# Optimization experiments

Hardware: AMD Instinct MI355X
Metric: run time of the kernel (lower is better)

Reference implementation:

```python
import jax, jax.numpy as jnp
import numpy as np

N, K = 8192, 16          # nodes, neighbours per node
FEAT = 128               # size + 1 (attention input dim)
DIST = 128               # distance_size (query dim & block width)
H, D = 8, 128            # heads, per-head attention size
HID = 128                # MLP hidden size
SCALE = 1.0 / np.sqrt(D)


def _lin_init(k, i, o):
    return jax.random.normal(k, (i, o), jnp.float32) / np.sqrt(i)


def setup_inputs() -> dict:
    key = jax.random.key(0)
    ks = jax.random.split(key, 12)
    z = lambda n: jnp.zeros((n,), jnp.float32)
    return {
        "features": jax.random.normal(ks[0], (N, FEAT), jnp.float32),
        "distance_features": jax.random.normal(ks[1], (N, DIST), jnp.float32),
        "structure": jax.random.randint(ks[2], (N, K), 0, N, jnp.int32),
        # attention projections
        "Wq": _lin_init(ks[3], DIST, H * D), "bq": z(H * D),
        "Wk": _lin_init(ks[4], FEAT, H * D), "bk": z(H * D),
        "Wv": _lin_init(ks[5], FEAT, H * D), "bv": z(H * D),
        "Wo": _lin_init(ks[6], H * D, DIST), "bo": z(DIST),
        # local MLP: depth=3 hidden layers + output layer
        "W1": _lin_init(ks[7], DIST, HID), "b1": z(HID),
        "W2": _lin_init(ks[8], HID, HID), "b2": z(HID),
        "W3": _lin_init(ks[9], HID, HID), "b3": z(HID),
        "W4": _lin_init(ks[10], HID, DIST), "b4": z(DIST),
    }


def reference(features, distance_features, structure,
              Wq, bq, Wk, bk, Wv, bv, Wo, bo,
              W1, b1, W2, b2, W3, b3, W4, b4):
    # bn / local_bn are identity (batch_norm=False); dropout identity (eval)
    normed = distance_features

    # NeighbourDotMultiHeadAttention: queries from distance feats, K/V from node feats
    q = (normed @ Wq + bq).reshape(N, H, D)
    k = (features @ Wk + bk).reshape(N, H, D)
    v = (features @ Wv + bv).reshape(N, H, D)
    kg = k[structure]                                  # [N, K, H, D] neighbour keys
    vg = v[structure]                                  # [N, K, H, D] neighbour values
    logits = jnp.einsum('nhd,nkhd->nkh', q, kg) * SCALE
    attn = jax.nn.softmax(logits, axis=1)              # over K neighbours
    att = jnp.einsum('nkh,nkhd->nhd', attn, vg).reshape(N, H * D)
    att_out = att @ Wo + bo                            # [N, DIST]

    out = distance_features + att_out                  # residual 1

    # local MLP with relu activations
    h = jax.nn.relu(out @ W1 + b1)
    h = jax.nn.relu(h @ W2 + b2)
    h = jax.nn.relu(h @ W3 + b3)
    mlp = h @ W4 + b4

    return out + mlp                                   # residual 2
```

## Files before the change

kernel.cpp:

```cpp
#include <hip/hip_runtime.h>
#include <hip/hip_bf16.h>

typedef float f32x4 __attribute__((ext_vector_type(4)));
typedef short s16x8 __attribute__((ext_vector_type(8)));
typedef unsigned short u16;

#define N_NODES 8192
#define KNBR 16
#define SCALE 0.08838834764831845f

__device__ __forceinline__ float bf2f(u16 h) {
    unsigned v = ((unsigned)h) << 16;
    return __builtin_bit_cast(float, v);
}
__device__ __forceinline__ u16 f2bf(float f) {
    unsigned u = __builtin_bit_cast(unsigned, f);
    u += 0x7fffu + ((u >> 16) & 1u);
    return (u16)(u >> 16);
}

__global__ void prep_kernel(const float* __restrict__ feat, const float* __restrict__ dist,
                            const float* __restrict__ Wq, const float* __restrict__ Wk,
                            const float* __restrict__ Wv, const float* __restrict__ Wo,
                            const float* __restrict__ W1, const float* __restrict__ W2,
                            const float* __restrict__ W3, const float* __restrict__ W4,
                            const float* __restrict__ bq, const float* __restrict__ bk,
                            const float* __restrict__ bv,
                            u16* __restrict__ featb, u16* __restrict__ distb,
                            u16* __restrict__ Wqkvt, u16* __restrict__ Wot,
                            u16* __restrict__ Wmlpt, float* __restrict__ bqkv) {
    int gid = blockIdx.x * 256 + threadIdx.x;
    featb[gid] = f2bf(feat[gid]);
    distb[gid] = f2bf(dist[gid]);
    if (gid < 3072 * 128) {
        int col = gid >> 7, k = gid & 127;
        float v = (col < 1024) ? Wq[k * 1024 + col]
                : (col < 2048) ? Wk[k * 1024 + (col - 1024)]
                               : Wv[k * 1024 + (col - 2048)];
        Wqkvt[gid] = f2bf(v);
    }
    if (gid < 128 * 1024) {
        int col = gid >> 10, k = gid & 1023;
        Wot[gid] = f2bf(Wo[k * 128 + col]);
    }
    if (gid < 4 * 128 * 128) {
        int m = gid >> 14, r = gid & 16383;
        int col = r >> 7, k = r & 127;
        const float* Wm = (m == 0) ? W1 : (m == 1) ? W2 : (m == 2) ? W3 : W4;
        Wmlpt[gid] = f2bf(Wm[k * 128 + col]);
    }
    if (gid < 3072) {
        bqkv[gid] = (gid < 1024) ? bq[gid] : (gid < 2048) ? bk[gid - 1024] : bv[gid - 2048];
    }
}

__global__ __launch_bounds__(256) void qkv_gemm(const u16* __restrict__ featb,
                                                const u16* __restrict__ distb,
                                                const u16* __restrict__ Wqkvt,
                                                const float* __restrict__ bqkv,
                                                u16* __restrict__ qkvh) {
    const int rt = blockIdx.x, ct = blockIdx.y;
    const int w = threadIdx.x >> 6, l = threadIdx.x & 63;
    const int rbase = rt * 64 + w * 16;
    const int cbase = ct * 128;
    const u16* A = (cbase < 1024) ? distb : featb;

    const u16* arow = A + (size_t)(rbase + (l & 15)) * 128 + ((l >> 4) * 8);

    f32x4 acc[8];
#pragma unroll
    for (int i = 0; i < 8; i++) acc[i] = (f32x4){0.f, 0.f, 0.f, 0.f};

#pragma unroll
    for (int kk = 0; kk < 4; kk++) {
        s16x8 af = *(const s16x8*)(arow + kk * 32);
#pragma unroll
        for (int nf = 0; nf < 8; nf++) {
            const u16* bp = Wqkvt + (size_t)(cbase + nf * 16 + (l & 15)) * 128
                          + kk * 32 + ((l >> 4) * 8);
            s16x8 bf = *(const s16x8*)bp;
            acc[nf] = __builtin_amdgcn_mfma_f32_16x16x32_bf16(af, bf, acc[nf], 0, 0, 0);
        }
    }
#pragma unroll
    for (int nf = 0; nf < 8; nf++) {
        const int gcol = cbase + nf * 16 + (l & 15);
        const float bias = bqkv[gcol];
        const int s = gcol >> 10;
        const int c = gcol & 1023;
        const int head = c >> 7, d = c & 127;
#pragma unroll
        for (int r = 0; r < 4; r++) {
            const int grow = rbase + (l >> 4) * 4 + r;
            qkvh[((size_t)(s * 8 + head) * 8192 + grow) * 128 + d] = f2bf(acc[nf][r] + bias);
        }
    }
}

__global__ __launch_bounds__(256) void attn_kernel(const u16* __restrict__ qkvh,
                                                   const int* __restrict__ structure,
                                                   u16* __restrict__ attb) {
    const int head = blockIdx.x & 7, chunk = blockIdx.x >> 3;
    const int w = threadIdx.x >> 6, l = threadIdx.x & 63;
    const int ni = l >> 3, lh = l & 7;
    const int n = chunk * 32 + w * 8 + ni;

    const u16* qrow = qkvh + ((size_t)(0 * 8 + head) * 8192 + n) * 128 + lh * 16;
    float qf[16];
    {
        s16x8 q0 = *(const s16x8*)qrow;
        s16x8 q1 = *(const s16x8*)(qrow + 8);
#pragma unroll
        for (int t = 0; t < 8; t++) { qf[t] = bf2f((u16)q0[t]); qf[8 + t] = bf2f((u16)q1[t]); }
    }

    const int2 idx2 = ((const int2*)structure)[n * 8 + lh];

    const u16* kbase = qkvh + (size_t)(1 * 8 + head) * 8192 * 128;
    const u16* vbase = qkvh + (size_t)(2 * 8 + head) * 8192 * 128;

    float logit[16];
#pragma unroll
    for (int j = 0; j < 16; j++) {
        int idx = __shfl(j & 1 ? idx2.y : idx2.x, (ni << 3) | (j >> 1));
        const u16* krow = kbase + (size_t)idx * 128 + lh * 16;
        s16x8 k0 = *(const s16x8*)krow;
        s16x8 k1 = *(const s16x8*)(krow + 8);
        float s = 0.f;
#pragma unroll
        for (int t = 0; t < 8; t++) {
            s += qf[t] * bf2f((u16)k0[t]);
            s += qf[8 + t] * bf2f((u16)k1[t]);
        }
        s += __shfl_xor(s, 1);
        s += __shfl_xor(s, 2);
        s += __shfl_xor(s, 4);
        logit[j] = s * SCALE;
    }

    float m = logit[0];
#pragma unroll
    for (int j = 1; j < 16; j++) m = fmaxf(m, logit[j]);
    float sum = 0.f;
#pragma unroll
    for (int j = 0; j < 16; j++) { logit[j] = __expf(logit[j] - m); sum += logit[j]; }
    const float inv = 1.f / sum;

    float acc[16];
#pragma unroll
    for (int t = 0; t < 16; t++) acc[t] = 0.f;
#pragma unroll
    for (int j = 0; j < 16; j++) {
        int idx = __shfl(j & 1 ? idx2.y : idx2.x, (ni << 3) | (j >> 1));
        const u16* vrow = vbase + (size_t)idx * 128 + lh * 16;
        s16x8 v0 = *(const s16x8*)vrow;
        s16x8 v1 = *(const s16x8*)(vrow + 8);
        const float p = logit[j] * inv;
#pragma unroll
        for (int t = 0; t < 8; t++) {
            acc[t]     += p * bf2f((u16)v0[t]);
            acc[8 + t] += p * bf2f((u16)v1[t]);
        }
    }

    s16x8 o0, o1;
#pragma unroll
    for (int t = 0; t < 8; t++) { o0[t] = (short)f2bf(acc[t]); o1[t] = (short)f2bf(acc[8 + t]); }
    u16* orow = attb + (size_t)n * 1024 + head * 128 + lh * 16;
    *(s16x8*)orow = o0;
    *(s16x8*)(orow + 8) = o1;
}

__global__ __launch_bounds__(64) void out_mlp(const u16* __restrict__ attb,
                                              const u16* __restrict__ Wot,
                                              const u16* __restrict__ Wmlpt,
                                              const float* __restrict__ dist,
                                              const float* __restrict__ bo,
                                              const float* __restrict__ b1,
                                              const float* __restrict__ b2,
                                              const float* __restrict__ b3,
                                              const float* __restrict__ b4,
                                              float* __restrict__ out) {
    __shared__ __attribute__((aligned(16))) u16 act[2][16][136];
    const int l = threadIdx.x & 63;
    const int rbase = blockIdx.x * 16;

    f32x4 acc[8];
#pragma unroll
    for (int i = 0; i < 8; i++) acc[i] = (f32x4){0.f, 0.f, 0.f, 0.f};

    const u16* ap = attb + (size_t)(rbase + (l & 15)) * 1024 + ((l >> 4) * 8);
#pragma unroll 4
    for (int kk = 0; kk < 32; kk++) {
        s16x8 af = *(const s16x8*)(ap + kk * 32);
#pragma unroll
        for (int nf = 0; nf < 8; nf++) {
            const u16* bp = Wot + (size_t)(nf * 16 + (l & 15)) * 1024 + kk * 32 + ((l >> 4) * 8);
            s16x8 bf = *(const s16x8*)bp;
            acc[nf] = __builtin_amdgcn_mfma_f32_16x16x32_bf16(af, bf, acc[nf], 0, 0, 0);
        }
    }

    float outsave[8][4];
#pragma unroll
    for (int nf = 0; nf < 8; nf++) {
        const int gcol = nf * 16 + (l & 15);
        const float bv = bo[gcol];
#pragma unroll
        for (int r = 0; r < 4; r++) {
            const int rl = (l >> 4) * 4 + r;
            float v = acc[nf][r] + bv + dist[(size_t)(rbase + rl) * 128 + gcol];
            outsave[nf][r] = v;
            act[0][rl][gcol] = f2bf(v);
        }
    }

#pragma unroll
    for (int layer = 0; layer < 4; layer++) {
        const int rd = layer & 1, wr = (layer + 1) & 1;
        f32x4 macc[8];
#pragma unroll
        for (int i = 0; i < 8; i++) macc[i] = (f32x4){0.f, 0.f, 0.f, 0.f};
#pragma unroll
        for (int kk = 0; kk < 4; kk++) {
            s16x8 af = *(const s16x8*)&act[rd][l & 15][kk * 32 + ((l >> 4) * 8)];
#pragma unroll
            for (int nf = 0; nf < 8; nf++) {
                const u16* bp = Wmlpt + layer * 16384
                              + (size_t)(nf * 16 + (l & 15)) * 128 + kk * 32 + ((l >> 4) * 8);
                s16x8 bf = *(const s16x8*)bp;
                macc[nf] = __builtin_amdgcn_mfma_f32_16x16x32_bf16(af, bf, macc[nf], 0, 0, 0);
            }
        }
        const float* bias = (layer == 0) ? b1 : (layer == 1) ? b2 : (layer == 2) ? b3 : b4;
        if (layer < 3) {
#pragma unroll
            for (int nf = 0; nf < 8; nf++) {
                const int gcol = nf * 16 + (l & 15);
                const float bv = bias[gcol];
#pragma unroll
                for (int r = 0; r < 4; r++) {
                    const int rl = (l >> 4) * 4 + r;
                    act[wr][rl][gcol] = f2bf(fmaxf(macc[nf][r] + bv, 0.f));
                }
            }
        } else {
#pragma unroll
            for (int nf = 0; nf < 8; nf++) {
                const int gcol = nf * 16 + (l & 15);
                const float bv = bias[gcol];
#pragma unroll
                for (int r = 0; r < 4; r++) {
                    const int rl = (l >> 4) * 4 + r;
                    out[(size_t)(rbase + rl) * 128 + gcol] = outsave[nf][r] + macc[nf][r] + bv;
                }
            }
        }
    }
}

extern "C" void kernel_launch(void* const* d_in, const int* in_sizes, int n_in,
                              void* d_out, int out_size, void* d_ws, size_t ws_size,
                              hipStream_t stream) {
    const float* features = (const float*)d_in[0];
    const float* dist     = (const float*)d_in[1];
    const int*   structure= (const int*)d_in[2];
    const float* Wq = (const float*)d_in[3];  const float* bq = (const float*)d_in[4];
    const float* Wk = (const float*)d_in[5];  const float* bk = (const float*)d_in[6];
    const float* Wv = (const float*)d_in[7];  const float* bv = (const float*)d_in[8];
    const float* Wo = (const float*)d_in[9];  const float* bo = (const float*)d_in[10];
    const float* W1 = (const float*)d_in[11]; const float* b1 = (const float*)d_in[12];
    const float* W2 = (const float*)d_in[13]; const float* b2 = (const float*)d_in[14];
    const float* W3 = (const float*)d_in[15]; const float* b3 = (const float*)d_in[16];
    const float* W4 = (const float*)d_in[17]; const float* b4 = (const float*)d_in[18];
    float* out = (float*)d_out;

    u16* wsp   = (u16*)d_ws;
    u16* qkvh  = wsp;
    u16* attb  = qkvh  + (size_t)3 * 8 * 8192 * 128;
    u16* featb = attb  + (size_t)8192 * 1024;
    u16* distb = featb + (size_t)8192 * 128;
    u16* Wqkvt = distb + (size_t)8192 * 128;
    u16* Wot   = Wqkvt + (size_t)3072 * 128;
    u16* Wmlpt = Wot   + (size_t)128 * 1024;
    float* bqkv = (float*)(Wmlpt + (size_t)4 * 128 * 128);

    prep_kernel<<<4096, 256, 0, stream>>>(features, dist, Wq, Wk, Wv, Wo, W1, W2, W3, W4,
                                          bq, bk, bv, featb, distb, Wqkvt, Wot, Wmlpt, bqkv);
    qkv_gemm<<<dim3(128, 24), 256, 0, stream>>>(featb, distb, Wqkvt, bqkv, qkvh);
    attn_kernel<<<2048, 256, 0, stream>>>(qkvh, structure, attb);
    out_mlp<<<512, 64, 0, stream>>>(attb, Wot, Wmlpt, dist, bo, b1, b2, b3, b4, out);
}
```

Before: 228.3 us.

## Enlarge QKV GEMM row tiles and split out_mlp columns across two waves

The QKV projection GEMM now gives each wave a 64x128 output tile. A fragments are held in registers and each B fragment is reused across four row fragments, which cuts redundant weight loads and uses a quarter of the blocks. The out_mlp kernel moves from one wave per 16-row block to two waves, each computing 64 output columns, with barriers between MLP layers because the shared activations are now split across waves. The bf16 conversion helper now uses the library intrinsic. The changes add register pressure in the GEMM and synchronisation cost in the MLP.

```diff
diff --git a/kernel.cpp b/kernel.cpp
--- a/kernel.cpp
+++ b/kernel.cpp
@@ -14,9 +14,8 @@
     return __builtin_bit_cast(float, v);
 }
 __device__ __forceinline__ u16 f2bf(float f) {
-    unsigned u = __builtin_bit_cast(unsigned, f);
-    u += 0x7fffu + ((u >> 16) & 1u);
-    return (u16)(u >> 16);
+    __hip_bfloat16 h = __float2bfloat16(f);
+    return __builtin_bit_cast(u16, h);
 }
 
 __global__ void prep_kernel(const float* __restrict__ feat, const float* __restrict__ dist,
@@ -54,45 +53,61 @@
     }
 }
 
-__global__ __launch_bounds__(256) void qkv_gemm(const u16* __restrict__ featb,
-                                                const u16* __restrict__ distb,
-                                                const u16* __restrict__ Wqkvt,
-                                                const float* __restrict__ bqkv,
-                                                u16* __restrict__ qkvh) {
+__global__ __launch_bounds__(256, 2) void qkv_gemm(const u16* __restrict__ featb,
+                                                   const u16* __restrict__ distb,
+                                                   const u16* __restrict__ Wqkvt,
+                                                   const float* __restrict__ bqkv,
+                                                   u16* __restrict__ qkvh) {
     const int rt = blockIdx.x, ct = blockIdx.y;
     const int w = threadIdx.x >> 6, l = threadIdx.x & 63;
-    const int rbase = rt * 64 + w * 16;
+    const int rbase = rt * 256 + w * 64;
     const int cbase = ct * 128;
-    const u16* A = (cbase < 1024) ? distb : featb;
-
-    const u16* arow = A + (size_t)(rbase + (l & 15)) * 128 + ((l >> 4) * 8);
-
-    f32x4 acc[8];
-#pragma unroll
-    for (int i = 0; i < 8; i++) acc[i] = (f32x4){0.f, 0.f, 0.f, 0.f};
-
-#pragma unroll
-    for (int kk = 0; kk < 4; kk++) {
-        s16x8 af = *(const s16x8*)(arow + kk * 32);
+    const u16* A = (ct < 8) ? distb : featb;
+
+    s16x8 af[4][4];
+#pragma unroll
+    for (int mf = 0; mf < 4; mf++) {
+        const u16* ar = A + (size_t)(rbase + mf * 16 + (l & 15)) * 128 + ((l >> 4) * 8);
+#pragma unroll
+        for (int kk = 0; kk < 4; kk++) af[mf][kk] = *(const s16x8*)(ar + kk * 32);
+    }
+
+    f32x4 acc[4][8];
+#pragma unroll
+    for (int mf = 0; mf < 4; mf++)
+#pragma unroll
+        for (int nf = 0; nf < 8; nf++) acc[mf][nf] = (f32x4){0.f, 0.f, 0.f, 0.f};
+
+#pragma unroll
+    for (int nf = 0; nf < 8; nf++) {
+        const u16* bp = Wqkvt + (size_t)(cbase + nf * 16 + (l & 15)) * 128 + ((l >> 4) * 8);
+        s16x8 b0 = *(const s16x8*)bp;
+        s16x8 b1 = *(const s16x8*)(bp + 32);
+        s16x8 b2 = *(const s16x8*)(bp + 64);
+        s16x8 b3 = *(const s16x8*)(bp + 96);
+#pragma unroll
+        for (int mf = 0; mf < 4; mf++) {
+            acc[mf][nf] = __builtin_amdgcn_mfma_f32_16x16x32_bf16(af[mf][0], b0, acc[mf][nf], 0, 0, 0);
+            acc[mf][nf] = __builtin_amdgcn_mfma_f32_16x16x32_bf16(af[mf][1], b1, acc[mf][nf], 0, 0, 0);
+            acc[mf][nf] = __builtin_amdgcn_mfma_f32_16x16x32_bf16(af[mf][2], b2, acc[mf][nf], 0, 0, 0);
+            acc[mf][nf] = __builtin_amdgcn_mfma_f32_16x16x32_bf16(af[mf][3], b3, acc[mf][nf], 0, 0, 0);
+        }
+    }
+
+    float bias[8];
+#pragma unroll
+    for (int nf = 0; nf < 8; nf++) bias[nf] = bqkv[cbase + nf * 16 + (l & 15)];
+
+    u16* obase = qkvh + ((size_t)ct * 8192 + rbase) * 128 + (l & 15);
+#pragma unroll
+    for (int mf = 0; mf < 4; mf++) {
 #pragma unroll
         for (int nf = 0; nf < 8; nf++) {
-            const u16* bp = Wqkvt + (size_t)(cbase + nf * 16 + (l & 15)) * 128
-                          + kk * 32 + ((l >> 4) * 8);
-            s16x8 bf = *(const s16x8*)bp;
-            acc[nf] = __builtin_amdgcn_mfma_f32_16x16x32_bf16(af, bf, acc[nf], 0, 0, 0);
-        }
-    }
-#pragma unroll
-    for (int nf = 0; nf < 8; nf++) {
-        const int gcol = cbase + nf * 16 + (l & 15);
-        const float bias = bqkv[gcol];
-        const int s = gcol >> 10;
-        const int c = gcol & 1023;
-        const int head = c >> 7, d = c & 127;
-#pragma unroll
-        for (int r = 0; r < 4; r++) {
-            const int grow = rbase + (l >> 4) * 4 + r;
-            qkvh[((size_t)(s * 8 + head) * 8192 + grow) * 128 + d] = f2bf(acc[nf][r] + bias);
+#pragma unroll
+            for (int r = 0; r < 4; r++) {
+                const int row = mf * 16 + (l >> 4) * 4 + r;
+                obase[(size_t)row * 128 + nf * 16] = f2bf(acc[mf][nf][r] + bias[nf]);
+            }
         }
     }
 }
@@ -171,40 +186,41 @@
     *(s16x8*)(orow + 8) = o1;
 }
 
-__global__ __launch_bounds__(64) void out_mlp(const u16* __restrict__ attb,
-                                              const u16* __restrict__ Wot,
-                                              const u16* __restrict__ Wmlpt,
-                                              const float* __restrict__ dist,
-                                              const float* __restrict__ bo,
-                                              const float* __restrict__ b1,
-                                              const float* __restrict__ b2,
-                                              const float* __restrict__ b3,
-                                              const float* __restrict__ b4,
-                                              float* __restrict__ out) {
+__global__ __launch_bounds__(128) void out_mlp(const u16* __restrict__ attb,
+                                               const u16* __restrict__ Wot,
+                                               const u16* __restrict__ Wmlpt,
+                                               const float* __restrict__ dist,
+                                               const float* __restrict__ bo,
+                                               const float* __restrict__ b1,
+                                               const float* __restrict__ b2,
+                                               const float* __restrict__ b3,
+                                               const float* __restrict__ b4,
+                                               float* __restrict__ out) {
     __shared__ __attribute__((aligned(16))) u16 act[2][16][136];
-    const int l = threadIdx.x & 63;
+    const int w = threadIdx.x >> 6, l = threadIdx.x & 63;
     const int rbase = blockIdx.x * 16;
-
-    f32x4 acc[8];
-#pragma unroll
-    for (int i = 0; i < 8; i++) acc[i] = (f32x4){0.f, 0.f, 0.f, 0.f};
+    const int cb = w * 64;
+
+    f32x4 acc[4];
+#pragma unroll
+    for (int i = 0; i < 4; i++) acc[i] = (f32x4){0.f, 0.f, 0.f, 0.f};
 
     const u16* ap = attb + (size_t)(rbase + (l & 15)) * 1024 + ((l >> 4) * 8);
 #pragma unroll 4
     for (int kk = 0; kk < 32; kk++) {
         s16x8 af = *(const s16x8*)(ap + kk * 32);
 #pragma unroll
-        for (int nf = 0; nf < 8; nf++) {
-            const u16* bp = Wot + (size_t)(nf * 16 + (l & 15)) * 1024 + kk * 32 + ((l >> 4) * 8);
+        for (int nf = 0; nf < 4; nf++) {
+            const u16* bp = Wot + (size_t)(cb + nf * 16 + (l & 15)) * 1024 + kk * 32 + ((l >> 4) * 8);
             s16x8 bf = *(const s16x8*)bp;
             acc[nf] = __builtin_amdgcn_mfma_f32_16x16x32_bf16(af, bf, acc[nf], 0, 0, 0);
         }
     }
 
-    float outsave[8][4];
-#pragma unroll
-    for (int nf = 0; nf < 8; nf++) {
-        const int gcol = nf * 16 + (l & 15);
+    float outsave[4][4];
+#pragma unroll
+    for (int nf = 0; nf < 4; nf++) {
+        const int gcol = cb + nf * 16 + (l & 15);
         const float bv = bo[gcol];
 #pragma unroll
         for (int r = 0; r < 4; r++) {
@@ -214,20 +230,21 @@
             act[0][rl][gcol] = f2bf(v);
         }
     }
+    __syncthreads();
 
 #pragma unroll
     for (int layer = 0; layer < 4; layer++) {
         const int rd = layer & 1, wr = (layer + 1) & 1;
-        f32x4 macc[8];
-#pragma unroll
-        for (int i = 0; i < 8; i++) macc[i] = (f32x4){0.f, 0.f, 0.f, 0.f};
+        f32x4 macc[4];
+#pragma unroll
+        for (int i = 0; i < 4; i++) macc[i] = (f32x4){0.f, 0.f, 0.f, 0.f};
 #pragma unroll
         for (int kk = 0; kk < 4; kk++) {
             s16x8 af = *(const s16x8*)&act[rd][l & 15][kk * 32 + ((l >> 4) * 8)];
 #pragma unroll
-            for (int nf = 0; nf < 8; nf++) {
+            for (int nf = 0; nf < 4; nf++) {
                 const u16* bp = Wmlpt + layer * 16384
-                              + (size_t)(nf * 16 + (l & 15)) * 128 + kk * 32 + ((l >> 4) * 8);
+                              + (size_t)(cb + nf * 16 + (l & 15)) * 128 + kk * 32 + ((l >> 4) * 8);
                 s16x8 bf = *(const s16x8*)bp;
                 macc[nf] = __builtin_amdgcn_mfma_f32_16x16x32_bf16(af, bf, macc[nf], 0, 0, 0);
             }
@@ -235,8 +252,8 @@
         const float* bias = (layer == 0) ? b1 : (layer == 1) ? b2 : (layer == 2) ? b3 : b4;
         if (layer < 3) {
 #pragma unroll
-            for (int nf = 0; nf < 8; nf++) {
-                const int gcol = nf * 16 + (l & 15);
+            for (int nf = 0; nf < 4; nf++) {
+                const int gcol = cb + nf * 16 + (l & 15);
                 const float bv = bias[gcol];
 #pragma unroll
                 for (int r = 0; r < 4; r++) {
@@ -244,10 +261,11 @@
                     act[wr][rl][gcol] = f2bf(fmaxf(macc[nf][r] + bv, 0.f));
                 }
             }
+            __syncthreads();
         } else {
 #pragma unroll
-            for (int nf = 0; nf < 8; nf++) {
-                const int gcol = nf * 16 + (l & 15);
+            for (int nf = 0; nf < 4; nf++) {
+                const int gcol = cb + nf * 16 + (l & 15);
                 const float bv = bias[gcol];
 #pragma unroll
                 for (int r = 0; r < 4; r++) {
@@ -287,7 +305,7 @@
 
     prep_kernel<<<4096, 256, 0, stream>>>(features, dist, Wq, Wk, Wv, Wo, W1, W2, W3, W4,
                                           bq, bk, bv, featb, distb, Wqkvt, Wot, Wmlpt, bqkv);
-    qkv_gemm<<<dim3(128, 24), 256, 0, stream>>>(featb, distb, Wqkvt, bqkv, qkvh);
+    qkv_gemm<<<dim3(32, 24), 256, 0, stream>>>(featb, distb, Wqkvt, bqkv, qkvh);
     attn_kernel<<<2048, 256, 0, stream>>>(qkvh, structure, attb);
-    out_mlp<<<512, 64, 0, stream>>>(attb, Wot, Wmlpt, dist, bo, b1, b2, b3, b4, out);
-}
+    out_mlp<<<512, 128, 0, stream>>>(attb, Wot, Wmlpt, dist, bo, b1, b2, b3, b4, out);
+}
```

Measured after the change: 189.6 us. 1.2x faster.
